# Kernel tuning notes

Measured on AMD Instinct MI355X. Metric: run time of the kernel, lower is better.

The kernel has to match this reference:

```python
import jax, jax.numpy as jnp
from jax import lax
import numpy as np

D_MODEL = 1024
D_STATE = 16
D_CONV = 4
EXPAND = 2
D_INNER = EXPAND * D_MODEL
IN_DIM = 256
OUT_DIM = 256
B = 2
T = 1024
LN_EPS = 1e-5


def setup_inputs() -> dict:
    key = jax.random.key(0)
    ks = jax.random.split(key, 10)
    s = lambda k, shape: (jax.random.normal(k, shape, dtype=jnp.float32) * 0.02)
    inp = {}
    inp["x"] = jax.random.normal(ks[0], (B, T, IN_DIM), dtype=jnp.float32)
    inp["hidden_state"] = jnp.zeros((B, D_INNER, D_STATE), dtype=jnp.float32)
    # wrapper input projection (Linear with bias)
    inp["W_in_wrap"] = s(ks[1], (IN_DIM, D_MODEL))
    inp["b_in_wrap"] = jnp.zeros((D_MODEL,), jnp.float32)
    # LayerNorm
    inp["ln_gamma"] = jnp.ones((D_MODEL,), jnp.float32)
    inp["ln_beta"] = jnp.zeros((D_MODEL,), jnp.float32)
    # Mamba block params
    inp["W_in"] = s(ks[2], (D_MODEL, 2 * D_INNER))          # in_proj, no bias
    inp["conv_w"] = s(ks[3], (D_INNER, 1, D_CONV))           # depthwise conv kernel (O,I/G,K)
    inp["conv_b"] = jnp.zeros((D_INNER,), jnp.float32)
    inp["W_x"] = s(ks[4], (D_INNER, 2 * D_STATE + D_INNER))  # x_proj, no bias
    inp["W_dt"] = s(ks[5], (D_INNER, D_INNER))
    inp["b_dt"] = jnp.zeros((D_INNER,), jnp.float32)
    A = jnp.tile(jnp.arange(1, D_STATE + 1, dtype=jnp.float32)[None, :], (D_INNER, 1))
    inp["A_log"] = jnp.log(A)
    inp["D_skip"] = jnp.ones((D_INNER,), jnp.float32)
    inp["W_out"] = s(ks[6], (D_INNER, D_MODEL))              # out_proj, no bias
    # wrapper output projection (Linear with bias)
    inp["W_out_wrap"] = s(ks[7], (D_MODEL, OUT_DIM))
    inp["b_out_wrap"] = jnp.zeros((OUT_DIM,), jnp.float32)
    return inp


def _silu(x):
    return x * jax.nn.sigmoid(x)


def _layernorm(x, gamma, beta):
    mu = jnp.mean(x, axis=-1, keepdims=True)
    var = jnp.mean(jnp.square(x - mu), axis=-1, keepdims=True)
    return (x - mu) * lax.rsqrt(var + LN_EPS) * gamma + beta


def _mamba_forward(x, hidden_state, W_in_wrap, b_in_wrap, ln_gamma, ln_beta,
                   W_in, conv_w, conv_b, W_x, W_dt, b_dt, A_log, D_skip,
                   W_out, W_out_wrap, b_out_wrap):
    # wrapper: input projection + layernorm
    h = x @ W_in_wrap + b_in_wrap            # [B,T,d_model]
    h = _layernorm(h, ln_gamma, ln_beta)

    # Mamba block
    xz = h @ W_in                             # [B,T,2*d_inner]
    x_branch, z = jnp.split(xz, 2, axis=-1)

    # causal depthwise conv1d (torch pads both sides by d_conv-1, slices to seq_len == left-pad only)
    xc = lax.conv_general_dilated(
        x_branch.transpose(0, 2, 1),          # [B, d_inner, T]
        conv_w,                               # [d_inner, 1, K]
        window_strides=(1,),
        padding=[(D_CONV - 1, 0)],
        feature_group_count=D_INNER,
        dimension_numbers=('NCH', 'OIH', 'NCH'))
    xc = xc + conv_b[None, :, None]
    u = _silu(xc.transpose(0, 2, 1))          # [B,T,d_inner]

    proj = u @ W_x                            # [B,T,2n+d_inner]
    B_in = proj[..., :D_STATE]                # [B,T,n]
    C_in = proj[..., D_STATE:2 * D_STATE]     # [B,T,n]
    dt = jax.nn.softplus(proj[..., 2 * D_STATE:] @ W_dt + b_dt)  # [B,T,d_inner]

    A = -jnp.exp(A_log)                       # [d_inner,n]
    dA = jnp.exp(dt[..., None] * A)                              # [B,T,d,n]
    dBu = dt[..., None] * B_in[:, :, None, :] * u[..., None]     # [B,T,d,n]

    def step(h_c, inputs):
        dA_t, dBu_t, C_t = inputs             # [B,d,n],[B,d,n],[B,n]
        h_c = dA_t * h_c + dBu_t
        y_t = jnp.einsum('bdn,bn->bd', h_c, C_t)
        return h_c, y_t

    hT, ys = lax.scan(step, hidden_state,
                      (dA.transpose(1, 0, 2, 3), dBu.transpose(1, 0, 2, 3), C_in.transpose(1, 0, 2)))
    y = ys.transpose(1, 0, 2)                 # [B,T,d_inner]
    y = y + u * D_skip
    y = y * _silu(z)
    out = (y @ W_out) @ W_out_wrap + b_out_wrap
    return out, hT


def reference(x, hidden_state, W_in_wrap, b_in_wrap, ln_gamma, ln_beta,
              W_in, conv_w, conv_b, W_x, W_dt, b_dt, A_log, D_skip,
              W_out, W_out_wrap, b_out_wrap):
    return _mamba_forward(x, hidden_state, W_in_wrap, b_in_wrap, ln_gamma, ln_beta,
                          W_in, conv_w, conv_b, W_x, W_dt, b_dt, A_log, D_skip,
                          W_out, W_out_wrap, b_out_wrap)
```

## Files before the change

### kernel.cpp

```cpp
#include <hip/hip_runtime.h>
#include <cstddef>
#include <cstdint>

#define D_MODEL 1024
#define D_STATE 16
#define D_CONV 4
#define D_INNER 2048
#define IN_DIM 256
#define OUT_DIM 256
#define BATCH 2
#define SEQ 1024
#define NTOK (BATCH*SEQ)
#define PROJ_N (2*D_STATE + D_INNER)
#define CHUNK 32
#define NCHUNK (SEQ/CHUNK)

typedef __attribute__((ext_vector_type(8))) short bf16x8;
typedef __attribute__((ext_vector_type(4))) float f32x4;

__device__ __forceinline__ float siluf(float x){ return x / (1.f + __expf(-x)); }

__device__ __forceinline__ unsigned short f2bf(float f) {
  uint32_t x = __float_as_uint(f);
  uint32_t r = x + 0x7fffu + ((x >> 16) & 1u);
  return (unsigned short)(r >> 16);
}
__device__ __forceinline__ float bf2f(unsigned short u) {
  return __uint_as_float(((uint32_t)u) << 16);
}

__device__ __forceinline__ void gload16(const void* g, void* l) {
  __builtin_amdgcn_global_load_lds((const __attribute__((address_space(1))) void*)g,
                                   (__attribute__((address_space(3))) void*)l, 16, 0, 0);
}

template<int k, typename T, int N>
__device__ __forceinline__ T (&pick4(T (&a)[N], T (&b)[N], T (&c)[N], T (&d)[N]))[N] {
  if constexpr (k == 0) return a; else if constexpr (k == 1) return b;
  else if constexpr (k == 2) return c; else return d;
}

__device__ __forceinline__ void tc_tile(float (*tile)[33], const float* __restrict__ in,
                                        unsigned short* __restrict__ out,
                                        int R, int C, int tcx, int tcy, int tid)
{
  const int bc = tcx * 32, br = tcy * 32;
  const int tx = tid & 31, ty = tid >> 5;
  #pragma unroll
  for (int i = 0; i < 4; ++i) {
    int r = ty + i*8;
    tile[r][tx] = in[(size_t)(br + r)*C + bc + tx];
  }
  __syncthreads();
  const int otx = tid & 7, oty = tid >> 3;
  ushort4 v;
  v.x = f2bf(tile[otx*4+0][oty]);
  v.y = f2bf(tile[otx*4+1][oty]);
  v.z = f2bf(tile[otx*4+2][oty]);
  v.w = f2bf(tile[otx*4+3][oty]);
  *(ushort4*)&out[(size_t)(bc + oty)*R + br + otx*4] = v;
}

__global__ __launch_bounds__(256)
void prep_k(const float* __restrict__ x, const float* __restrict__ Wiw,
            const float* __restrict__ Win, const float* __restrict__ Wx,
            const float* __restrict__ Wdt, const float* __restrict__ Wout,
            const float* __restrict__ Wwr,
            unsigned short* __restrict__ xb16, unsigned short* __restrict__ WiwT,
            unsigned short* __restrict__ WinT, unsigned short* __restrict__ WxT,
            unsigned short* __restrict__ WdtT, unsigned short* __restrict__ Wob,
            unsigned short* __restrict__ WwrT)
{
  __shared__ float tile[32][33];
  const int tid = threadIdx.x;
  int id = blockIdx.x;
  if (id < 4096)  { tc_tile(tile, Win,  WinT,  1024, 4096, id % 128, id / 128, tid); return; }
  id -= 4096;
  if (id < 4160)  { tc_tile(tile, Wx,   WxT,   2048, 2080, id % 65,  id / 65,  tid); return; }
  id -= 4160;
  if (id < 4096)  { tc_tile(tile, Wdt,  WdtT,  2048, 2048, id % 64,  id / 64,  tid); return; }
  id -= 4096;
  if (id < 2048) {
    int i = id * 256 + tid;
    float4 v = ((const float4*)Wout)[i];
    ushort4 o;
    o.x = f2bf(v.x); o.y = f2bf(v.y); o.z = f2bf(v.z); o.w = f2bf(v.w);
    ((ushort4*)Wob)[i] = o;
    return;
  }
  id -= 2048;
  if (id < 256)   { tc_tile(tile, Wwr,  WwrT,  1024, 256,  id % 8,   id / 8,   tid); return; }
  id -= 256;
  if (id < 256)   { tc_tile(tile, Wiw,  WiwT,  256,  1024, id % 32,  id / 32,  tid); return; }
  id -= 256;
  if (id < 512) {
    int i = id * 256 + tid;
    float4 v = ((const float4*)x)[i];
    ushort4 o;
    o.x = f2bf(v.x); o.y = f2bf(v.y); o.z = f2bf(v.z); o.w = f2bf(v.w);
    ((ushort4*)xb16)[i] = o;
    return;
  }
  id -= 512;
  {
    unsigned short* p = WxT + (size_t)(2080 + id) * 2048 + tid * 8;
    ushort4 z = {0,0,0,0};
    *(ushort4*)p = z; *(ushort4*)(p + 4) = z;
  }
}

template<int MODE>
__global__ __launch_bounds__(512)
void gemm2ph(const unsigned short* __restrict__ A, const unsigned short* __restrict__ B,
             int M, int N, int K, int lda, int ldb,
             const float* __restrict__ bias,
             void* __restrict__ out0, void* __restrict__ out1)
{
  __shared__ __align__(1024) unsigned short S[2][256*64];
  const int tid = threadIdx.x;
  const int lane = tid & 63, w = tid >> 6;
  const int row0 = blockIdx.y * 128, col0 = blockIdx.x * 128;
  const int wr = (w >> 2) * 64, wc = (w & 3) * 32;
  const int l15 = lane & 15, lg4 = lane >> 4;

  int afo[4][2], bfo[2][2];
  #pragma unroll
  for (int fi = 0; fi < 4; ++fi)
    #pragma unroll
    for (int h = 0; h < 2; ++h) {
      const int r = wr + fi*16 + l15;
      const int q = h*4 + lg4;
      afo[fi][h] = r*64 + (q ^ (r & 7))*8;
    }
  #pragma unroll
  for (int fj = 0; fj < 2; ++fj)
    #pragma unroll
    for (int h = 0; h < 2; ++h) {
      const int r = wc + fj*16 + l15;
      const int q = h*4 + lg4;
      bfo[fj][h] = (128 + r)*64 + (q ^ (r & 7))*8;
    }

  const unsigned short* src[4];
  int dsto[4];
  #pragma unroll
  for (int i = 0; i < 4; ++i) {
    const int base = w*32 + i*8;
    const int row = base + (lane >> 3);
    const int gs = (lane & 7) ^ (row & 7);
    dsto[i] = base*64;
    src[i] = (row < 128) ? A + (size_t)(row0 + row) * lda + gs*8
                         : B + (size_t)(col0 + row - 128) * ldb + gs*8;
  }

  f32x4 acc[4][2];
  #pragma unroll
  for (int i=0;i<4;i++)
    #pragma unroll
    for (int j=0;j<2;j++) acc[i][j] = (f32x4){0.f,0.f,0.f,0.f};

  const int NT = K >> 6;

  auto stage = [&](int buf) {
    #pragma unroll
    for (int i = 0; i < 4; ++i) { gload16(src[i], &S[buf][dsto[i]]); src[i] += 64; }
  };

  stage(0);
  asm volatile("s_waitcnt vmcnt(0)" ::: "memory");
  __builtin_amdgcn_s_barrier();
  asm volatile("" ::: "memory");

  int cur = 0;
  for (int t = 0; t < NT; ++t) {
    if (t + 1 < NT) stage(cur ^ 1);
    #pragma unroll
    for (int h = 0; h < 2; ++h) {
      bf16x8 af[4], bfv[2];
      #pragma unroll
      for (int fi = 0; fi < 4; ++fi) af[fi] = *(const bf16x8*)&S[cur][afo[fi][h]];
      #pragma unroll
      for (int fj = 0; fj < 2; ++fj) bfv[fj] = *(const bf16x8*)&S[cur][bfo[fj][h]];
      __builtin_amdgcn_s_setprio(1);
      #pragma unroll
      for (int fi = 0; fi < 4; ++fi)
        #pragma unroll
        for (int fj = 0; fj < 2; ++fj)
          acc[fi][fj] = __builtin_amdgcn_mfma_f32_16x16x32_bf16(af[fi], bfv[fj], acc[fi][fj], 0, 0, 0);
      __builtin_amdgcn_s_setprio(0);
    }
    asm volatile("s_waitcnt vmcnt(0) lgkmcnt(0)" ::: "memory");
    __builtin_amdgcn_s_barrier();
    asm volatile("" ::: "memory");
    cur ^= 1;
  }

  #pragma unroll
  for (int fi=0; fi<4; fi++){
    const int rb = row0 + wr + fi*16 + lg4*4;
    #pragma unroll
    for (int fj=0; fj<2; fj++){
      const int c = col0 + wc + fj*16 + l15;
      #pragma unroll
      for (int q=0;q<4;q++){
        const int r = rb + q;
        float v = acc[fi][fj][q];
        if constexpr (MODE == 1) {
          if (c < N) { v += bias[c]; v = (v > 20.f) ? v : log1pf(__expf(v));
                       ((float*)out0)[(size_t)r*N + c] = v; }
        } else if constexpr (MODE == 3) {
          if (c < 2048) ((float*)out0)[(size_t)r*2048 + c] = v;
          else          ((unsigned short*)out1)[(size_t)r*2048 + (c - 2048)] = f2bf(v);
        } else {
          if (c < 32) ((float*)out0)[(size_t)r*32 + c] = v;
          else if (c < N) ((unsigned short*)out1)[(size_t)r*2048 + (c - 32)] = f2bf(v);
        }
      }
    }
  }
}

template<int BM, int BN, int MODE>
__global__ __launch_bounds__(256)
void gemm_bf16(const unsigned short* __restrict__ A, const unsigned short* __restrict__ B,
               int M, int N, int K, int lda, int ldb,
               const float* __restrict__ bias,
               void* __restrict__ out0, void* __restrict__ out1)
{
  constexpr int FM = BM / 32;
  constexpr int FN = BN / 32;
  constexpr int ROWS = BM + BN;
  constexpr int GR = ROWS / 64;
  __shared__ __align__(1024) unsigned short S[2][ROWS*32];

  const int tid = threadIdx.x;
  const int lane = tid & 63, w = tid >> 6;
  const int row0 = blockIdx.y * BM, col0 = blockIdx.x * BN;
  const int wr = (w >> 1) * (BM/2), wc = (w & 1) * (BN/2);
  const int l15 = lane & 15, lg4 = lane >> 4;

  size_t zoff = 0;
  if constexpr (MODE == 5) {
    A += (size_t)blockIdx.z * (size_t)K;
    B += (size_t)blockIdx.z * (size_t)K;
    zoff = (size_t)blockIdx.z * (size_t)(gridDim.y * BM) * (size_t)N;
  }

  int afo[FM], bfo[FN];
  #pragma unroll
  for (int fi = 0; fi < FM; ++fi) {
    const int r = wr + fi*16 + l15;
    afo[fi] = r*32 + (lg4 ^ ((r >> 1) & 3))*8;
  }
  #pragma unroll
  for (int fj = 0; fj < FN; ++fj) {
    const int r = wc + fj*16 + l15;
    bfo[fj] = (BM + r)*32 + (lg4 ^ ((r >> 1) & 3))*8;
  }

  const unsigned short* src[GR];
  int ldso[GR];
  #pragma unroll
  for (int i = 0; i < GR; ++i) {
    const int g = tid + i*256;
    const int row = g >> 2, q = g & 3;
    ldso[i] = row*32 + (q ^ ((row >> 1) & 3))*8;
    src[i] = (row < BM) ? A + (size_t)(row0 + row) * lda + q*8
                        : B + (size_t)(col0 + row - BM) * ldb + q*8;
  }

  f32x4 acc[FM][FN];
  #pragma unroll
  for (int i=0;i<FM;i++)
    #pragma unroll
    for (int j=0;j<FN;j++) acc[i][j] = (f32x4){0.f,0.f,0.f,0.f};

  const int NT = K >> 5;
  bf16x8 g0[GR], g1[GR], g2[GR], g3[GR];

  auto loadg = [&](bf16x8 (&g)[GR]) {
    #pragma unroll
    for (int i = 0; i < GR; ++i) { g[i] = *(const bf16x8*)src[i]; src[i] += 32; }
  };

  loadg(g0); loadg(g1); loadg(g2); loadg(g3);
  #pragma unroll
  for (int i = 0; i < GR; ++i) *(bf16x8*)(&S[0][ldso[i]]) = g0[i];
  asm volatile("s_waitcnt lgkmcnt(0)" ::: "memory");
  __builtin_amdgcn_s_barrier();
  asm volatile("" ::: "memory");

#define STEP(I) do {                                                          \
    const int j = base + (I);                                                 \
    if (j < NT) {                                                             \
      bf16x8 af[FM], bfv[FN];                                                 \
      _Pragma("unroll")                                                       \
      for (int fi = 0; fi < FM; ++fi)                                         \
        af[fi] = *(const bf16x8*)&S[(I)&1][afo[fi]];                          \
      _Pragma("unroll")                                                       \
      for (int fj = 0; fj < FN; ++fj)                                         \
        bfv[fj] = *(const bf16x8*)&S[(I)&1][bfo[fj]];                         \
      if (j + 4 < NT) loadg(pick4<(I)&3>(g0, g1, g2, g3));                    \
      _Pragma("unroll")                                                       \
      for (int fi = 0; fi < FM; ++fi)                                         \
        _Pragma("unroll")                                                     \
        for (int fj = 0; fj < FN; ++fj)                                       \
          acc[fi][fj] = __builtin_amdgcn_mfma_f32_16x16x32_bf16(              \
              af[fi], bfv[fj], acc[fi][fj], 0, 0, 0);                         \
      if (j + 1 < NT) {                                                       \
        bf16x8 (&gw)[GR] = pick4<((I)+1)&3>(g0, g1, g2, g3);                  \
        _Pragma("unroll")                                                     \
        for (int i = 0; i < GR; ++i)                                          \
          *(bf16x8*)(&S[((I)+1)&1][ldso[i]]) = gw[i];                         \
      }                                                                       \
      asm volatile("s_waitcnt lgkmcnt(0)" ::: "memory");                      \
      __builtin_amdgcn_s_barrier();                                           \
      asm volatile("" ::: "memory");                                          \
    }                                                                         \
  } while (0)

  for (int base = 0; base < NT; base += 4) {
    STEP(0); STEP(1); STEP(2); STEP(3);
  }
#undef STEP

  #pragma unroll
  for (int fi=0; fi<FM; fi++){
    const int rb = row0 + wr + fi*16 + lg4*4;
    #pragma unroll
    for (int fj=0; fj<FN; fj++){
      const int c = col0 + wc + fj*16 + l15;
      #pragma unroll
      for (int q=0;q<4;q++){
        const int r = rb + q;
        float v = acc[fi][fj][q];
        if constexpr (MODE == 0) {
          if (c < N) ((float*)out0)[(size_t)r*N + c] = bias ? v + bias[c] : v;
        } else if constexpr (MODE == 2) {
          if (c < N) ((unsigned short*)out0)[(size_t)r*N + c] = f2bf(v);
        } else {
          if (c < N) ((float*)out0)[zoff + (size_t)r*N + c] = v;
        }
      }
    }
  }
}

__global__ __launch_bounds__(256)
void red4_wf(const float* __restrict__ p, unsigned short* __restrict__ out)
{
  const size_t S = (size_t)256*2048;
  const int i = (blockIdx.x * 256 + threadIdx.x) * 4;
  float4 a = *(const float4*)(p + i);
  float4 b = *(const float4*)(p + S + i);
  float4 c = *(const float4*)(p + 2*S + i);
  float4 d = *(const float4*)(p + 3*S + i);
  ushort4 o;
  o.x = f2bf(a.x+b.x+c.x+d.x);
  o.y = f2bf(a.y+b.y+c.y+d.y);
  o.z = f2bf(a.z+b.z+c.z+d.z);
  o.w = f2bf(a.w+b.w+c.w+d.w);
  *(ushort4*)(out + i) = o;
}

__global__ __launch_bounds__(256)
void red4_out(const float* __restrict__ p, const float* __restrict__ bias,
              float* __restrict__ out)
{
  const size_t S = (size_t)2048*256;
  const int i = (blockIdx.x * 256 + threadIdx.x) * 4;
  float4 a = *(const float4*)(p + i);
  float4 b = *(const float4*)(p + S + i);
  float4 c = *(const float4*)(p + 2*S + i);
  float4 d = *(const float4*)(p + 3*S + i);
  float4 bb = *(const float4*)(bias + (i & 255));
  float4 o;
  o.x = a.x+b.x+c.x+d.x + bb.x;
  o.y = a.y+b.y+c.y+d.y + bb.y;
  o.z = a.z+b.z+c.z+d.z + bb.z;
  o.w = a.w+b.w+c.w+d.w + bb.w;
  *(float4*)(out + i) = o;
}

__global__ __launch_bounds__(256)
void ln_k(const float* __restrict__ h, const float* __restrict__ gamma,
          const float* __restrict__ beta, unsigned short* __restrict__ hb)
{
  const int row = blockIdx.x;
  const float* p = h + (size_t)row * D_MODEL;
  float s = 0.f, s2 = 0.f;
  for (int i = threadIdx.x; i < D_MODEL; i += 256) { float v = p[i]; s += v; s2 += v*v; }
  #pragma unroll
  for (int off = 32; off; off >>= 1) { s += __shfl_down(s, off, 64); s2 += __shfl_down(s2, off, 64); }
  __shared__ float ss[4], ss2[4];
  __shared__ float smu, sinv;
  const int wid = threadIdx.x >> 6;
  if ((threadIdx.x & 63) == 0) { ss[wid] = s; ss2[wid] = s2; }
  __syncthreads();
  if (threadIdx.x == 0) {
    float S = ss[0]+ss[1]+ss[2]+ss[3];
    float S2 = ss2[0]+ss2[1]+ss2[2]+ss2[3];
    float mu = S * (1.f / D_MODEL);
    float var = S2 * (1.f / D_MODEL) - mu * mu;
    smu = mu; sinv = rsqrtf(var + 1e-5f);
  }
  __syncthreads();
  const float mu = smu, inv = sinv;
  unsigned short* q = hb + (size_t)row * D_MODEL;
  for (int i = threadIdx.x; i < D_MODEL; i += 256)
    q[i] = f2bf((p[i] - mu) * inv * gamma[i] + beta[i]);
}

__global__ __launch_bounds__(256)
void conv_silu_k(const float* __restrict__ xb, const float* __restrict__ cw,
                 const float* __restrict__ cb, unsigned short* __restrict__ ub)
{
  const int idx = blockIdx.x * 256 + threadIdx.x;
  const int d4 = (idx & 511) * 4;
  const int bt = idx >> 9;
  const int t  = bt & (SEQ - 1);
  float4 acc = *(const float4*)(cb + d4);
  const float* base = xb + (size_t)bt * D_INNER + d4;
  #pragma unroll
  for (int k = 0; k < D_CONV; ++k) {
    int tt = t + k - (D_CONV - 1);
    if (tt >= 0) {
      float4 xv = *(const float4*)(base + (ptrdiff_t)(k - (D_CONV-1)) * D_INNER);
      acc.x = fmaf(cw[(d4+0)*D_CONV + k], xv.x, acc.x);
      acc.y = fmaf(cw[(d4+1)*D_CONV + k], xv.y, acc.y);
      acc.z = fmaf(cw[(d4+2)*D_CONV + k], xv.z, acc.z);
      acc.w = fmaf(cw[(d4+3)*D_CONV + k], xv.w, acc.w);
    }
  }
  ushort4 o;
  o.x = f2bf(siluf(acc.x)); o.y = f2bf(siluf(acc.y));
  o.z = f2bf(siluf(acc.z)); o.w = f2bf(siluf(acc.w));
  *(ushort4*)(ub + (size_t)bt * D_INNER + d4) = o;
}

__global__ __launch_bounds__(256)
void scan_p1(const float* __restrict__ dtb, const unsigned short* __restrict__ ub,
             const float* __restrict__ BC, const float* __restrict__ A_log,
             float* __restrict__ summ)
{
  const int bid = blockIdx.x;
  const int b = bid >> 8;
  const int c = (bid >> 3) & (NCHUNK - 1);
  const int d = ((bid & 7) << 8) + threadIdx.x;
  float A[D_STATE], hl[D_STATE];
  #pragma unroll
  for (int n = 0; n < D_STATE; ++n) { A[n] = -__expf(A_log[d*D_STATE + n]); hl[n] = 0.f; }
  float dtsum = 0.f;
  const size_t row0 = (size_t)b * SEQ + (size_t)c * CHUNK;
  float dtv = dtb[row0*D_INNER + d];
  float uv  = bf2f(ub[row0*D_INNER + d]);
  float Bv[D_STATE];
  #pragma unroll
  for (int n = 0; n < D_STATE; ++n) Bv[n] = BC[row0*32 + n];
  for (int t = 0; t < CHUNK; ++t) {
    const size_t rn = row0 + ((t+1 < CHUNK) ? (t+1) : t);
    float ndt = dtb[rn*D_INNER + d];
    float nu  = bf2f(ub[rn*D_INNER + d]);
    float nB[D_STATE];
    #pragma unroll
    for (int n = 0; n < D_STATE; ++n) nB[n] = BC[rn*32 + n];
    const float du = dtv * uv;
    dtsum += dtv;
    #pragma unroll
    for (int n = 0; n < D_STATE; ++n) {
      float dA = __expf(dtv * A[n]);
      hl[n] = fmaf(dA, hl[n], du * Bv[n]);
    }
    dtv = ndt; uv = nu;
    #pragma unroll
    for (int n = 0; n < D_STATE; ++n) Bv[n] = nB[n];
  }
  float* s = summ + (((size_t)b*NCHUNK + c)*32)*D_INNER + d;
  #pragma unroll
  for (int n = 0; n < D_STATE; ++n) {
    s[(size_t)n*D_INNER]      = __expf(A[n] * dtsum);
    s[(size_t)(16+n)*D_INNER] = hl[n];
  }
}

__global__ __launch_bounds__(256)
void scan_p2(float* __restrict__ summ, const float* __restrict__ h0,
             float* __restrict__ outH)
{
  const int b = blockIdx.x >> 3;
  const int d = ((blockIdx.x & 7) << 8) + threadIdx.x;
  float h[D_STATE];
  #pragma unroll
  for (int n = 0; n < D_STATE; ++n) h[n] = h0[((size_t)b*D_INNER + d)*D_STATE + n];
  float pv[D_STATE], lv[D_STATE];
  float* s0 = summ + (((size_t)b*NCHUNK + 0)*32)*D_INNER + d;
  #pragma unroll
  for (int n = 0; n < D_STATE; ++n) { pv[n] = s0[(size_t)n*D_INNER]; lv[n] = s0[(size_t)(16+n)*D_INNER]; }
  for (int c = 0; c < NCHUNK; ++c) {
    float* s = summ + (((size_t)b*NCHUNK + c)*32)*D_INNER + d;
    const int cn = (c+1 < NCHUNK) ? (c+1) : c;
    float* sn = summ + (((size_t)b*NCHUNK + cn)*32)*D_INNER + d;
    float np[D_STATE], nl[D_STATE];
    #pragma unroll
    for (int n = 0; n < D_STATE; ++n) { np[n] = sn[(size_t)n*D_INNER]; nl[n] = sn[(size_t)(16+n)*D_INNER]; }
    #pragma unroll
    for (int n = 0; n < D_STATE; ++n) {
      s[(size_t)n*D_INNER] = h[n];
      h[n] = fmaf(pv[n], h[n], lv[n]);
      pv[n] = np[n]; lv[n] = nl[n];
    }
  }
  #pragma unroll
  for (int n = 0; n < D_STATE; ++n)
    outH[((size_t)b*D_INNER + d)*D_STATE + n] = h[n];
}

__global__ __launch_bounds__(256)
void scan_p3(const float* __restrict__ dtb, const unsigned short* __restrict__ ub,
             const unsigned short* __restrict__ zbh, const float* __restrict__ BC,
             const float* __restrict__ A_log, const float* __restrict__ D_skip,
             const float* __restrict__ summ, unsigned short* __restrict__ yb)
{
  const int bid = blockIdx.x;
  const int b = bid >> 8;
  const int c = (bid >> 3) & (NCHUNK - 1);
  const int d = ((bid & 7) << 8) + threadIdx.x;
  float A[D_STATE], h[D_STATE];
  const float* s = summ + (((size_t)b*NCHUNK + c)*32)*D_INNER + d;
  #pragma unroll
  for (int n = 0; n < D_STATE; ++n) {
    A[n] = -__expf(A_log[d*D_STATE + n]);
    h[n] = s[(size_t)n*D_INNER];
  }
  const float Ds = D_skip[d];
  const size_t row0 = (size_t)b * SEQ + (size_t)c * CHUNK;
  float dtv = dtb[row0*D_INNER + d];
  float uv  = bf2f(ub[row0*D_INNER + d]);
  float zv  = bf2f(zbh[row0*D_INNER + d]);
  float Bv[D_STATE], Cv[D_STATE];
  #pragma unroll
  for (int n = 0; n < D_STATE; ++n) { Bv[n] = BC[row0*32 + n]; Cv[n] = BC[row0*32 + 16 + n]; }
  for (int t = 0; t < CHUNK; ++t) {
    const size_t r = row0 + t;
    const size_t rn = row0 + ((t+1 < CHUNK) ? (t+1) : t);
    float ndt = dtb[rn*D_INNER + d];
    float nu  = bf2f(ub[rn*D_INNER + d]);
    float nz  = bf2f(zbh[rn*D_INNER + d]);
    float nB[D_STATE], nC[D_STATE];
    #pragma unroll
    for (int n = 0; n < D_STATE; ++n) { nB[n] = BC[rn*32 + n]; nC[n] = BC[rn*32 + 16 + n]; }
    const float du = dtv * uv;
    float y = 0.f;
    #pragma unroll
    for (int n = 0; n < D_STATE; ++n) {
      float dA = __expf(dtv * A[n]);
      h[n] = fmaf(dA, h[n], du * Bv[n]);
      y = fmaf(h[n], Cv[n], y);
    }
    y = fmaf(uv, Ds, y);
    yb[r*D_INNER + d] = f2bf(y * siluf(zv));
    dtv = ndt; uv = nu; zv = nz;
    #pragma unroll
    for (int n = 0; n < D_STATE; ++n) { Bv[n] = nB[n]; Cv[n] = nC[n]; }
  }
}

extern "C" void kernel_launch(void* const* d_in, const int* in_sizes, int n_in,
                              void* d_out, int out_size, void* d_ws, size_t ws_size,
                              hipStream_t stream) {
  const float* x          = (const float*)d_in[0];
  const float* h0         = (const float*)d_in[1];
  const float* W_in_wrap  = (const float*)d_in[2];
  const float* b_in_wrap  = (const float*)d_in[3];
  const float* ln_g       = (const float*)d_in[4];
  const float* ln_b       = (const float*)d_in[5];
  const float* W_in       = (const float*)d_in[6];
  const float* conv_w     = (const float*)d_in[7];
  const float* conv_b     = (const float*)d_in[8];
  const float* W_x        = (const float*)d_in[9];
  const float* W_dt       = (const float*)d_in[10];
  const float* b_dt       = (const float*)d_in[11];
  const float* A_log      = (const float*)d_in[12];
  const float* D_skip     = (const float*)d_in[13];
  const float* W_out      = (const float*)d_in[14];
  const float* W_out_wrap = (const float*)d_in[15];
  const float* b_out_wrap = (const float*)d_in[16];

  float* out  = (float*)d_out;
  float* outH = out + (size_t)NTOK * OUT_DIM;

  char* ws = (char*)d_ws;
  auto at = [&](size_t kb){ return (void*)(ws + kb*1024); };
  float*          hbuf = (float*)at(0);
  float*          wfp  = hbuf;
  float*          xb   = (float*)at(8192);
  float*          dtb  = xb;
  float*          outp = xb;
  unsigned short* zbh  = (unsigned short*)at(24576);
  unsigned short* WfT  = (unsigned short*)at(32768);
  unsigned short* ub   = (unsigned short*)at(40960);
  unsigned short* xb16 = ub;
  unsigned short* gb   = (unsigned short*)at(49152);
  unsigned short* WiwT = gb;
  unsigned short* yb   = gb;
  unsigned short* hb   = (unsigned short*)at(57344);
  float*          BC   = (float*)at(61440);
  unsigned short* WinT = (unsigned short*)at(61696);
  unsigned short* WxT  = (unsigned short*)at(69888);
  float*          summ = (float*)at(61696);
  unsigned short* WdtT = (unsigned short*)at(78592);
  unsigned short* Wob  = (unsigned short*)at(86784);
  unsigned short* WwrT = (unsigned short*)at(90880);

  dim3 blk(256);
  dim3 blk512(512);
  prep_k<<<dim3(15520), blk, 0, stream>>>(x, W_in_wrap, W_in, W_x, W_dt, W_out, W_out_wrap,
                                          xb16, WiwT, WinT, WxT, WdtT, Wob, WwrT);
  gemm_bf16<64,64,5><<<dim3(2048/64, 256/64, 4), blk, 0, stream>>>(WwrT, Wob, 256, 2048, 1024/4,
                                                                   1024, 1024, nullptr, wfp, nullptr);
  red4_wf<<<dim3(512), blk, 0, stream>>>(wfp, WfT);
  gemm_bf16<64,64,0><<<dim3(1024/64, NTOK/64), blk, 0, stream>>>(xb16, WiwT, NTOK, 1024, 256,
                                                                 256, 256, b_in_wrap, hbuf, nullptr);
  ln_k<<<dim3(NTOK), blk, 0, stream>>>(hbuf, ln_g, ln_b, hb);
  gemm2ph<3><<<dim3(4096/128, NTOK/128), blk512, 0, stream>>>(hb, WinT, NTOK, 4096, 1024,
                                                              1024, 1024, nullptr, xb, zbh);
  conv_silu_k<<<dim3(NTOK*D_INNER/4/256), blk, 0, stream>>>(xb, conv_w, conv_b, ub);
  gemm2ph<4><<<dim3(2176/128, NTOK/128), blk512, 0, stream>>>(ub, WxT, NTOK, PROJ_N, 2048,
                                                              2048, 2048, nullptr, BC, gb);
  gemm2ph<1><<<dim3(2048/128, NTOK/128), blk512, 0, stream>>>(gb, WdtT, NTOK, 2048, 2048,
                                                              2048, 2048, b_dt, dtb, nullptr);
  scan_p1<<<dim3(BATCH*NCHUNK*(D_INNER/256)), blk, 0, stream>>>(dtb, ub, BC, A_log, summ);
  scan_p2<<<dim3(BATCH*(D_INNER/256)), blk, 0, stream>>>(summ, h0, outH);
  scan_p3<<<dim3(BATCH*NCHUNK*(D_INNER/256)), blk, 0, stream>>>(dtb, ub, zbh, BC, A_log, D_skip, summ, yb);
  gemm_bf16<64,64,5><<<dim3(256/64, NTOK/64, 4), blk, 0, stream>>>(yb, WfT, NTOK, 256, 2048/4,
                                                                   2048, 2048, nullptr, outp, nullptr);
  red4_out<<<dim3(512), blk, 0, stream>>>(outp, b_out_wrap, out);
}
```

Before: 256.8 us.

## Add triple-buffered GEMM pipeline, halve scan chunk size, compact chunk summaries

Makes the 128x128 GEMM's pipeline depth a template parameter and adds a three-stage LDS ring with one barrier per K-step. The two K=2048 projection GEMMs use it, so global loads run two tiles ahead instead of one. The chunked scan moves from 32-token to 16-token chunks, doubling chunk-level parallelism in passes 1 and 3. Each chunk summary now stores the dt sum instead of 16 decay products, and pass 2 recomputes the exponentials. This trades more sequential work and extra exps in the serial pass 2, plus more LDS per GEMM block, for shorter serial chunks and less summary traffic.

```diff
diff --git a/kernel.cpp b/kernel.cpp
--- a/kernel.cpp
+++ b/kernel.cpp
@@ -12,7 +12,7 @@
 #define SEQ 1024
 #define NTOK (BATCH*SEQ)
 #define PROJ_N (2*D_STATE + D_INNER)
-#define CHUNK 32
+#define CHUNK 16
 #define NCHUNK (SEQ/CHUNK)
 
 typedef __attribute__((ext_vector_type(8))) short bf16x8;
@@ -109,14 +109,14 @@
   }
 }
 
-template<int MODE>
+template<int MODE, int DEPTH>
 __global__ __launch_bounds__(512)
 void gemm2ph(const unsigned short* __restrict__ A, const unsigned short* __restrict__ B,
              int M, int N, int K, int lda, int ldb,
              const float* __restrict__ bias,
              void* __restrict__ out0, void* __restrict__ out1)
 {
-  __shared__ __align__(1024) unsigned short S[2][256*64];
+  __shared__ __align__(1024) unsigned short S[DEPTH][256*64];
   const int tid = threadIdx.x;
   const int lane = tid & 63, w = tid >> 6;
   const int row0 = blockIdx.y * 128, col0 = blockIdx.x * 128;
@@ -165,22 +165,14 @@
     #pragma unroll
     for (int i = 0; i < 4; ++i) { gload16(src[i], &S[buf][dsto[i]]); src[i] += 64; }
   };
-
-  stage(0);
-  asm volatile("s_waitcnt vmcnt(0)" ::: "memory");
-  __builtin_amdgcn_s_barrier();
-  asm volatile("" ::: "memory");
-
-  int cur = 0;
-  for (int t = 0; t < NT; ++t) {
-    if (t + 1 < NT) stage(cur ^ 1);
+  auto compute = [&](const unsigned short* Sb) {
     #pragma unroll
     for (int h = 0; h < 2; ++h) {
       bf16x8 af[4], bfv[2];
       #pragma unroll
-      for (int fi = 0; fi < 4; ++fi) af[fi] = *(const bf16x8*)&S[cur][afo[fi][h]];
+      for (int fi = 0; fi < 4; ++fi) af[fi] = *(const bf16x8*)(Sb + afo[fi][h]);
       #pragma unroll
-      for (int fj = 0; fj < 2; ++fj) bfv[fj] = *(const bf16x8*)&S[cur][bfo[fj][h]];
+      for (int fj = 0; fj < 2; ++fj) bfv[fj] = *(const bf16x8*)(Sb + bfo[fj][h]);
       __builtin_amdgcn_s_setprio(1);
       #pragma unroll
       for (int fi = 0; fi < 4; ++fi)
@@ -189,10 +181,35 @@
           acc[fi][fj] = __builtin_amdgcn_mfma_f32_16x16x32_bf16(af[fi], bfv[fj], acc[fi][fj], 0, 0, 0);
       __builtin_amdgcn_s_setprio(0);
     }
-    asm volatile("s_waitcnt vmcnt(0) lgkmcnt(0)" ::: "memory");
+  };
+
+  if constexpr (DEPTH == 2) {
+    stage(0);
+    asm volatile("s_waitcnt vmcnt(0)" ::: "memory");
     __builtin_amdgcn_s_barrier();
     asm volatile("" ::: "memory");
-    cur ^= 1;
+    int cur = 0;
+    for (int t = 0; t < NT; ++t) {
+      if (t + 1 < NT) stage(cur ^ 1);
+      compute(&S[cur][0]);
+      asm volatile("s_waitcnt vmcnt(0) lgkmcnt(0)" ::: "memory");
+      __builtin_amdgcn_s_barrier();
+      asm volatile("" ::: "memory");
+      cur ^= 1;
+    }
+  } else {
+    stage(0);
+    if (NT > 1) stage(1);
+    int cur = 0;
+    for (int t = 0; t < NT; ++t) {
+      if (t + 1 < NT) asm volatile("s_waitcnt vmcnt(4)" ::: "memory");
+      else            asm volatile("s_waitcnt vmcnt(0)" ::: "memory");
+      __builtin_amdgcn_s_barrier();
+      asm volatile("" ::: "memory");
+      if (t + 2 < NT) stage((cur + 2) % 3);
+      compute(&S[cur][0]);
+      cur = (cur + 1) % 3;
+    }
   }
 
   #pragma unroll
@@ -444,7 +461,7 @@
              float* __restrict__ summ)
 {
   const int bid = blockIdx.x;
-  const int b = bid >> 8;
+  const int b = bid >> 9;
   const int c = (bid >> 3) & (NCHUNK - 1);
   const int d = ((bid & 7) << 8) + threadIdx.x;
   float A[D_STATE], hl[D_STATE];
@@ -475,40 +492,46 @@
     #pragma unroll
     for (int n = 0; n < D_STATE; ++n) Bv[n] = nB[n];
   }
-  float* s = summ + (((size_t)b*NCHUNK + c)*32)*D_INNER + d;
-  #pragma unroll
-  for (int n = 0; n < D_STATE; ++n) {
-    s[(size_t)n*D_INNER]      = __expf(A[n] * dtsum);
-    s[(size_t)(16+n)*D_INNER] = hl[n];
-  }
+  float* s = summ + (((size_t)b*NCHUNK + c)*17)*D_INNER + d;
+  s[0] = dtsum;
+  #pragma unroll
+  for (int n = 0; n < D_STATE; ++n)
+    s[(size_t)(1+n)*D_INNER] = hl[n];
 }
 
 __global__ __launch_bounds__(256)
 void scan_p2(float* __restrict__ summ, const float* __restrict__ h0,
-             float* __restrict__ outH)
+             const float* __restrict__ A_log, float* __restrict__ outH)
 {
   const int b = blockIdx.x >> 3;
   const int d = ((blockIdx.x & 7) << 8) + threadIdx.x;
-  float h[D_STATE];
-  #pragma unroll
-  for (int n = 0; n < D_STATE; ++n) h[n] = h0[((size_t)b*D_INNER + d)*D_STATE + n];
-  float pv[D_STATE], lv[D_STATE];
-  float* s0 = summ + (((size_t)b*NCHUNK + 0)*32)*D_INNER + d;
-  #pragma unroll
-  for (int n = 0; n < D_STATE; ++n) { pv[n] = s0[(size_t)n*D_INNER]; lv[n] = s0[(size_t)(16+n)*D_INNER]; }
+  float A[D_STATE], h[D_STATE];
+  #pragma unroll
+  for (int n = 0; n < D_STATE; ++n) {
+    A[n] = -__expf(A_log[d*D_STATE + n]);
+    h[n] = h0[((size_t)b*D_INNER + d)*D_STATE + n];
+  }
+  float dts, lv[D_STATE];
+  float* s0 = summ + (((size_t)b*NCHUNK + 0)*17)*D_INNER + d;
+  dts = s0[0];
+  #pragma unroll
+  for (int n = 0; n < D_STATE; ++n) lv[n] = s0[(size_t)(1+n)*D_INNER];
   for (int c = 0; c < NCHUNK; ++c) {
-    float* s = summ + (((size_t)b*NCHUNK + c)*32)*D_INNER + d;
+    float* s = summ + (((size_t)b*NCHUNK + c)*17)*D_INNER + d;
     const int cn = (c+1 < NCHUNK) ? (c+1) : c;
-    float* sn = summ + (((size_t)b*NCHUNK + cn)*32)*D_INNER + d;
-    float np[D_STATE], nl[D_STATE];
-    #pragma unroll
-    for (int n = 0; n < D_STATE; ++n) { np[n] = sn[(size_t)n*D_INNER]; nl[n] = sn[(size_t)(16+n)*D_INNER]; }
+    float* sn = summ + (((size_t)b*NCHUNK + cn)*17)*D_INNER + d;
+    float ndts = sn[0];
+    float nl[D_STATE];
+    #pragma unroll
+    for (int n = 0; n < D_STATE; ++n) nl[n] = sn[(size_t)(1+n)*D_INNER];
     #pragma unroll
     for (int n = 0; n < D_STATE; ++n) {
-      s[(size_t)n*D_INNER] = h[n];
-      h[n] = fmaf(pv[n], h[n], lv[n]);
-      pv[n] = np[n]; lv[n] = nl[n];
-    }
+      float p = __expf(A[n] * dts);
+      s[(size_t)(1+n)*D_INNER] = h[n];
+      h[n] = fmaf(p, h[n], lv[n]);
+      lv[n] = nl[n];
+    }
+    dts = ndts;
   }
   #pragma unroll
   for (int n = 0; n < D_STATE; ++n)
@@ -522,15 +545,15 @@
              const float* __restrict__ summ, unsigned short* __restrict__ yb)
 {
   const int bid = blockIdx.x;
-  const int b = bid >> 8;
+  const int b = bid >> 9;
   const int c = (bid >> 3) & (NCHUNK - 1);
   const int d = ((bid & 7) << 8) + threadIdx.x;
   float A[D_STATE], h[D_STATE];
-  const float* s = summ + (((size_t)b*NCHUNK + c)*32)*D_INNER + d;
+  const float* s = summ + (((size_t)b*NCHUNK + c)*17)*D_INNER + d;
   #pragma unroll
   for (int n = 0; n < D_STATE; ++n) {
     A[n] = -__expf(A_log[d*D_STATE + n]);
-    h[n] = s[(size_t)n*D_INNER];
+    h[n] = s[(size_t)(1+n)*D_INNER];
   }
   const float Ds = D_skip[d];
   const size_t row0 = (size_t)b * SEQ + (size_t)c * CHUNK;
@@ -622,15 +645,15 @@
   gemm_bf16<64,64,0><<<dim3(1024/64, NTOK/64), blk, 0, stream>>>(xb16, WiwT, NTOK, 1024, 256,
                                                                  256, 256, b_in_wrap, hbuf, nullptr);
   ln_k<<<dim3(NTOK), blk, 0, stream>>>(hbuf, ln_g, ln_b, hb);
-  gemm2ph<3><<<dim3(4096/128, NTOK/128), blk512, 0, stream>>>(hb, WinT, NTOK, 4096, 1024,
-                                                              1024, 1024, nullptr, xb, zbh);
+  gemm2ph<3,2><<<dim3(4096/128, NTOK/128), blk512, 0, stream>>>(hb, WinT, NTOK, 4096, 1024,
+                                                                1024, 1024, nullptr, xb, zbh);
   conv_silu_k<<<dim3(NTOK*D_INNER/4/256), blk, 0, stream>>>(xb, conv_w, conv_b, ub);
-  gemm2ph<4><<<dim3(2176/128, NTOK/128), blk512, 0, stream>>>(ub, WxT, NTOK, PROJ_N, 2048,
-                                                              2048, 2048, nullptr, BC, gb);
-  gemm2ph<1><<<dim3(2048/128, NTOK/128), blk512, 0, stream>>>(gb, WdtT, NTOK, 2048, 2048,
-                                                              2048, 2048, b_dt, dtb, nullptr);
+  gemm2ph<4,3><<<dim3(2176/128, NTOK/128), blk512, 0, stream>>>(ub, WxT, NTOK, PROJ_N, 2048,
+                                                                2048, 2048, nullptr, BC, gb);
+  gemm2ph<1,3><<<dim3(2048/128, NTOK/128), blk512, 0, stream>>>(gb, WdtT, NTOK, 2048, 2048,
+                                                                2048, 2048, b_dt, dtb, nullptr);
   scan_p1<<<dim3(BATCH*NCHUNK*(D_INNER/256)), blk, 0, stream>>>(dtb, ub, BC, A_log, summ);
-  scan_p2<<<dim3(BATCH*(D_INNER/256)), blk, 0, stream>>>(summ, h0, outH);
+  scan_p2<<<dim3(BATCH*(D_INNER/256)), blk, 0, stream>>>(summ, h0, A_log, outH);
   scan_p3<<<dim3(BATCH*NCHUNK*(D_INNER/256)), blk, 0, stream>>>(dtb, ub, zbh, BC, A_log, D_skip, summ, yb);
   gemm_bf16<64,64,5><<<dim3(256/64, NTOK/64, 4), blk, 0, stream>>>(yb, WfT, NTOK, 256, 2048/4,
                                                                    2048, 2048, nullptr, outp, nullptr);
```

Result: slower. 278.9 us (+8.6%).

## Halve scan chunk size and split chunk-state propagation into hierarchical three-pass scan

Applied to the files above, without the earlier changes.

Chunk length drops from 32 to 16, which doubles the number of chunks and the parallelism available to the per-chunk scan passes. The serial inter-chunk pass, previously one 16-block kernel walking all chunks, becomes three kernels: group summaries, a short serial scan over 8 groups, then per-group propagation. Chunk summaries now store only the dt sum and the local state, and the decay factor is recomputed with exp where it is needed. The cost is two extra kernel launches and extra exp work, in exchange for shorter serial dependency chains.

```diff
diff --git a/kernel.cpp b/kernel.cpp
--- a/kernel.cpp
+++ b/kernel.cpp
@@ -12,8 +12,10 @@
 #define SEQ 1024
 #define NTOK (BATCH*SEQ)
 #define PROJ_N (2*D_STATE + D_INNER)
-#define CHUNK 32
+#define CHUNK 16
 #define NCHUNK (SEQ/CHUNK)
+#define GROUPS 8
+#define GCH (NCHUNK/GROUPS)
 
 typedef __attribute__((ext_vector_type(8))) short bf16x8;
 typedef __attribute__((ext_vector_type(4))) float f32x4;
@@ -444,7 +446,7 @@
              float* __restrict__ summ)
 {
   const int bid = blockIdx.x;
-  const int b = bid >> 8;
+  const int b = bid >> 9;
   const int c = (bid >> 3) & (NCHUNK - 1);
   const int d = ((bid & 7) << 8) + threadIdx.x;
   float A[D_STATE], hl[D_STATE];
@@ -475,44 +477,96 @@
     #pragma unroll
     for (int n = 0; n < D_STATE; ++n) Bv[n] = nB[n];
   }
-  float* s = summ + (((size_t)b*NCHUNK + c)*32)*D_INNER + d;
-  #pragma unroll
-  for (int n = 0; n < D_STATE; ++n) {
-    s[(size_t)n*D_INNER]      = __expf(A[n] * dtsum);
-    s[(size_t)(16+n)*D_INNER] = hl[n];
-  }
-}
-
-__global__ __launch_bounds__(256)
-void scan_p2(float* __restrict__ summ, const float* __restrict__ h0,
-             float* __restrict__ outH)
+  float* s = summ + (((size_t)b*NCHUNK + c)*17)*D_INNER + d;
+  s[0] = dtsum;
+  #pragma unroll
+  for (int n = 0; n < D_STATE; ++n)
+    s[(size_t)(1+n)*D_INNER] = hl[n];
+}
+
+__global__ __launch_bounds__(256)
+void scan_p2a(const float* __restrict__ summ, const float* __restrict__ A_log,
+              float* __restrict__ gsum)
+{
+  const int bid = blockIdx.x;
+  const int b = bid >> 6;
+  const int g = (bid >> 3) & (GROUPS - 1);
+  const int d = ((bid & 7) << 8) + threadIdx.x;
+  float A[D_STATE], Lg[D_STATE];
+  #pragma unroll
+  for (int n = 0; n < D_STATE; ++n) { A[n] = -__expf(A_log[d*D_STATE + n]); Lg[n] = 0.f; }
+  float dtsg = 0.f;
+  for (int j = 0; j < GCH; ++j) {
+    const int c = g*GCH + j;
+    const float* s = summ + (((size_t)b*NCHUNK + c)*17)*D_INNER + d;
+    const float dts = s[0];
+    #pragma unroll
+    for (int n = 0; n < D_STATE; ++n) {
+      float p = __expf(A[n] * dts);
+      Lg[n] = fmaf(p, Lg[n], s[(size_t)(1+n)*D_INNER]);
+    }
+    dtsg += dts;
+  }
+  float* gs = gsum + (((size_t)b*GROUPS + g)*17)*D_INNER + d;
+  gs[0] = dtsg;
+  #pragma unroll
+  for (int n = 0; n < D_STATE; ++n)
+    gs[(size_t)(1+n)*D_INNER] = Lg[n];
+}
+
+__global__ __launch_bounds__(256)
+void scan_p2b(float* __restrict__ gsum, const float* __restrict__ h0,
+              const float* __restrict__ A_log, float* __restrict__ outH)
 {
   const int b = blockIdx.x >> 3;
   const int d = ((blockIdx.x & 7) << 8) + threadIdx.x;
-  float h[D_STATE];
-  #pragma unroll
-  for (int n = 0; n < D_STATE; ++n) h[n] = h0[((size_t)b*D_INNER + d)*D_STATE + n];
-  float pv[D_STATE], lv[D_STATE];
-  float* s0 = summ + (((size_t)b*NCHUNK + 0)*32)*D_INNER + d;
-  #pragma unroll
-  for (int n = 0; n < D_STATE; ++n) { pv[n] = s0[(size_t)n*D_INNER]; lv[n] = s0[(size_t)(16+n)*D_INNER]; }
-  for (int c = 0; c < NCHUNK; ++c) {
-    float* s = summ + (((size_t)b*NCHUNK + c)*32)*D_INNER + d;
-    const int cn = (c+1 < NCHUNK) ? (c+1) : c;
-    float* sn = summ + (((size_t)b*NCHUNK + cn)*32)*D_INNER + d;
-    float np[D_STATE], nl[D_STATE];
-    #pragma unroll
-    for (int n = 0; n < D_STATE; ++n) { np[n] = sn[(size_t)n*D_INNER]; nl[n] = sn[(size_t)(16+n)*D_INNER]; }
+  float A[D_STATE], h[D_STATE];
+  #pragma unroll
+  for (int n = 0; n < D_STATE; ++n) {
+    A[n] = -__expf(A_log[d*D_STATE + n]);
+    h[n] = h0[((size_t)b*D_INNER + d)*D_STATE + n];
+  }
+  for (int g = 0; g < GROUPS; ++g) {
+    float* gs = gsum + (((size_t)b*GROUPS + g)*17)*D_INNER + d;
+    const float dts = gs[0];
     #pragma unroll
     for (int n = 0; n < D_STATE; ++n) {
-      s[(size_t)n*D_INNER] = h[n];
-      h[n] = fmaf(pv[n], h[n], lv[n]);
-      pv[n] = np[n]; lv[n] = nl[n];
+      float L = gs[(size_t)(1+n)*D_INNER];
+      gs[(size_t)(1+n)*D_INNER] = h[n];
+      h[n] = fmaf(__expf(A[n] * dts), h[n], L);
     }
   }
   #pragma unroll
   for (int n = 0; n < D_STATE; ++n)
     outH[((size_t)b*D_INNER + d)*D_STATE + n] = h[n];
+}
+
+__global__ __launch_bounds__(256)
+void scan_p2c(float* __restrict__ summ, const float* __restrict__ gsum,
+              const float* __restrict__ A_log)
+{
+  const int bid = blockIdx.x;
+  const int b = bid >> 6;
+  const int g = (bid >> 3) & (GROUPS - 1);
+  const int d = ((bid & 7) << 8) + threadIdx.x;
+  float A[D_STATE], h[D_STATE];
+  const float* gs = gsum + (((size_t)b*GROUPS + g)*17)*D_INNER + d;
+  #pragma unroll
+  for (int n = 0; n < D_STATE; ++n) {
+    A[n] = -__expf(A_log[d*D_STATE + n]);
+    h[n] = gs[(size_t)(1+n)*D_INNER];
+  }
+  for (int j = 0; j < GCH; ++j) {
+    const int c = g*GCH + j;
+    float* s = summ + (((size_t)b*NCHUNK + c)*17)*D_INNER + d;
+    const float dts = s[0];
+    #pragma unroll
+    for (int n = 0; n < D_STATE; ++n) {
+      float hl = s[(size_t)(1+n)*D_INNER];
+      s[(size_t)(1+n)*D_INNER] = h[n];
+      h[n] = fmaf(__expf(A[n] * dts), h[n], hl);
+    }
+  }
 }
 
 __global__ __launch_bounds__(256)
@@ -522,15 +576,15 @@
              const float* __restrict__ summ, unsigned short* __restrict__ yb)
 {
   const int bid = blockIdx.x;
-  const int b = bid >> 8;
+  const int b = bid >> 9;
   const int c = (bid >> 3) & (NCHUNK - 1);
   const int d = ((bid & 7) << 8) + threadIdx.x;
   float A[D_STATE], h[D_STATE];
-  const float* s = summ + (((size_t)b*NCHUNK + c)*32)*D_INNER + d;
+  const float* s = summ + (((size_t)b*NCHUNK + c)*17)*D_INNER + d;
   #pragma unroll
   for (int n = 0; n < D_STATE; ++n) {
     A[n] = -__expf(A_log[d*D_STATE + n]);
-    h[n] = s[(size_t)n*D_INNER];
+    h[n] = s[(size_t)(1+n)*D_INNER];
   }
   const float Ds = D_skip[d];
   const size_t row0 = (size_t)b * SEQ + (size_t)c * CHUNK;
@@ -593,6 +647,7 @@
   auto at = [&](size_t kb){ return (void*)(ws + kb*1024); };
   float*          hbuf = (float*)at(0);
   float*          wfp  = hbuf;
+  float*          gsum = hbuf;
   float*          xb   = (float*)at(8192);
   float*          dtb  = xb;
   float*          outp = xb;
@@ -630,7 +685,9 @@
   gemm2ph<1><<<dim3(2048/128, NTOK/128), blk512, 0, stream>>>(gb, WdtT, NTOK, 2048, 2048,
                                                               2048, 2048, b_dt, dtb, nullptr);
   scan_p1<<<dim3(BATCH*NCHUNK*(D_INNER/256)), blk, 0, stream>>>(dtb, ub, BC, A_log, summ);
-  scan_p2<<<dim3(BATCH*(D_INNER/256)), blk, 0, stream>>>(summ, h0, outH);
+  scan_p2a<<<dim3(BATCH*GROUPS*(D_INNER/256)), blk, 0, stream>>>(summ, A_log, gsum);
+  scan_p2b<<<dim3(BATCH*(D_INNER/256)), blk, 0, stream>>>(gsum, h0, A_log, outH);
+  scan_p2c<<<dim3(BATCH*GROUPS*(D_INNER/256)), blk, 0, stream>>>(summ, gsum, A_log);
   scan_p3<<<dim3(BATCH*NCHUNK*(D_INNER/256)), blk, 0, stream>>>(dtb, ub, zbh, BC, A_log, D_skip, summ, yb);
   gemm_bf16<64,64,5><<<dim3(256/64, NTOK/64, 4), blk, 0, stream>>>(yb, WfT, NTOK, 256, 2048/4,
                                                                    2048, 2048, nullptr, outp, nullptr);
```

Result: faster. 241.9 us (-5.8%).
